# Kernel optimization log

Measured on AMD Instinct MI355X. Metric: run time of the kernel, lower is better.

## Reference

```python
import jax, jax.numpy as jnp
import numpy as np

N = 20000        # nodes
E = 640000       # edges (before self-loops)
F_IN = 128
HID = 64
HEADS = 4
F_OUT = 128
G = 64           # graphs in batch
NEG_SLOPE = 0.2  # PyG GATConv leaky_relu default


def setup_inputs() -> dict:
    key = jax.random.key(0)
    ks = jax.random.split(key, 16)
    s = 0.05
    x = jax.random.normal(ks[0], (N, F_IN), jnp.float32)
    edge_index = jax.random.randint(ks[1], (2, E), 0, N, dtype=jnp.int64)
    batch = jnp.sort(jax.random.randint(ks[2], (N,), 0, G, dtype=jnp.int64))
    # layer 1: F_IN -> HID x HEADS (concat)
    W1 = jax.random.normal(ks[3], (F_IN, HEADS * HID), jnp.float32) * s
    a_src1 = jax.random.normal(ks[4], (HEADS, HID), jnp.float32) * s
    a_dst1 = jax.random.normal(ks[5], (HEADS, HID), jnp.float32) * s
    b1 = jnp.zeros((HEADS * HID,), jnp.float32)
    # layer 2: HEADS*HID -> HID x HEADS (concat)
    W2 = jax.random.normal(ks[6], (HEADS * HID, HEADS * HID), jnp.float32) * s
    a_src2 = jax.random.normal(ks[7], (HEADS, HID), jnp.float32) * s
    a_dst2 = jax.random.normal(ks[8], (HEADS, HID), jnp.float32) * s
    b2 = jnp.zeros((HEADS * HID,), jnp.float32)
    # layer 3: HEADS*HID -> F_OUT, heads=1, concat=False (mean)
    W3 = jax.random.normal(ks[9], (HEADS * HID, F_OUT), jnp.float32) * s
    a_src3 = jax.random.normal(ks[10], (1, F_OUT), jnp.float32) * s
    a_dst3 = jax.random.normal(ks[11], (1, F_OUT), jnp.float32) * s
    b3 = jnp.zeros((F_OUT,), jnp.float32)
    return dict(x=x, edge_index=edge_index, batch=batch,
                W1=W1, a_src1=a_src1, a_dst1=a_dst1, b1=b1,
                W2=W2, a_src2=a_src2, a_dst2=a_dst2, b2=b2,
                W3=W3, a_src3=a_src3, a_dst3=a_dst3, b3=b3)


def _gat_layer(x, src, dst, W, a_s, a_d, b, heads, concat):
    n = x.shape[0]
    h = (x @ W).reshape(n, heads, -1)                # [N,H,C]
    alpha_s = (h * a_s[None]).sum(-1)                # [N,H]
    alpha_d = (h * a_d[None]).sum(-1)                # [N,H]
    e = jax.nn.leaky_relu(alpha_s[src] + alpha_d[dst], NEG_SLOPE)  # [E,H]
    # segment softmax over incoming edges of each dst node
    m = jax.ops.segment_max(e, dst, num_segments=n)
    ex = jnp.exp(e - m[dst])
    denom = jax.ops.segment_sum(ex, dst, num_segments=n)
    alpha = ex / (denom[dst] + 1e-16)                # [E,H]
    out = jax.ops.segment_sum(alpha[:, :, None] * h[src], dst, num_segments=n)  # [N,H,C]
    out = out.reshape(n, -1) if concat else out.mean(axis=1)
    return out + b


def reference(x, edge_index, batch, W1, a_src1, a_dst1, b1,
              W2, a_src2, a_dst2, b2, W3, a_src3, a_dst3, b3):
    n = x.shape[0]
    # add self loops (PyG GATConv default add_self_loops=True)
    loop = jnp.arange(n, dtype=edge_index.dtype)
    src = jnp.concatenate([edge_index[0], loop])
    dst = jnp.concatenate([edge_index[1], loop])

    h = _gat_layer(x, src, dst, W1, a_src1, a_dst1, b1, HEADS, True)
    h = jax.nn.elu(h)
    h = _gat_layer(h, src, dst, W2, a_src2, a_dst2, b2, HEADS, True)
    h = jax.nn.elu(h)
    h = _gat_layer(h, src, dst, W3, a_src3, a_dst3, b3, 1, False)

    # global mean pool over graphs
    sums = jax.ops.segment_sum(h, batch, num_segments=G)
    cnts = jax.ops.segment_sum(jnp.ones((n, 1), h.dtype), batch, num_segments=G)
    graph_embedding = sums / jnp.maximum(cnts, 1.0)
    return graph_embedding, h
```

## Files before the change

### kernel.cpp

```cpp
#include <hip/hip_runtime.h>
#include <hip/hip_bf16.h>
#include <math.h>

#define N_NODES 20000
#define N_EDGES 640000
#define ET_EDGES (N_EDGES + N_NODES)
#define G_GRAPHS 64
#define NEG_SLOPE 0.2f

typedef __attribute__((ext_vector_type(8))) short s8v;
typedef __attribute__((ext_vector_type(4))) float f4v;

__device__ __forceinline__ unsigned short bf_hi(float f) {
    union { float f; unsigned int u; } c; c.f = f;
    unsigned int r = (c.u + 0x7fffu + ((c.u >> 16) & 1u)) >> 16;
    return (unsigned short)r;
}
__device__ __forceinline__ float bf_f(unsigned short h) {
    union { unsigned int u; float f; } c; c.u = ((unsigned int)h) << 16;
    return c.f;
}


__global__ void hist_dst(const int* __restrict__ ei, int* __restrict__ cnt,
                         const int* __restrict__ batch, int* __restrict__ gstart) {
    int j = blockIdx.x * blockDim.x + threadIdx.x;
    if (blockIdx.x == 0 && threadIdx.x <= G_GRAPHS) {
        int g = threadIdx.x;
        int lo = 0, hi = N_NODES;
        while (lo < hi) {
            int mid = (lo + hi) >> 1;
            if (batch[mid] < g) lo = mid + 1; else hi = mid;
        }
        gstart[g] = lo;
    }
    if (j >= ET_EDGES) return;
    int d = (j < N_EDGES) ? ei[N_EDGES + j] : (j - N_EDGES);
    atomicAdd(&cnt[d], 1);
}

__global__ __launch_bounds__(1024) void scan_rowptr(const int* __restrict__ cnt,
                                                    int* __restrict__ row_ptr) {
    __shared__ int sums[1024];
    const int n = N_NODES;
    const int CH = (n + 1023) / 1024;
    int t = threadIdx.x;
    int base = t * CH;
    int s = 0;
    for (int i = 0; i < CH; ++i) {
        int idx = base + i;
        if (idx < n) s += cnt[idx];
    }
    sums[t] = s;
    __syncthreads();
    for (int o = 1; o < 1024; o <<= 1) {
        int v = (t >= o) ? sums[t - o] : 0;
        __syncthreads();
        sums[t] += v;
        __syncthreads();
    }
    int run = (t == 0) ? 0 : sums[t - 1];
    for (int i = 0; i < CH; ++i) {
        int idx = base + i;
        if (idx < n) { row_ptr[idx] = run; run += cnt[idx]; }
    }
    if (t == 1023) row_ptr[n] = sums[1023];
}

__global__ void fill_csr(const int* __restrict__ ei, const int* __restrict__ row_ptr,
                         int* __restrict__ cur, int* __restrict__ col) {
    int j = blockIdx.x * blockDim.x + threadIdx.x;
    if (j >= ET_EDGES) return;
    int s, d;
    if (j < N_EDGES) { s = ei[j]; d = ei[N_EDGES + j]; }
    else             { s = d = j - N_EDGES; }
    int pos = row_ptr[d] + atomicAdd(&cur[d], 1);
    col[pos] = s;
}


__global__ void prep_split(const float* __restrict__ x,
                           const float* __restrict__ W1, const float* __restrict__ W2,
                           const float* __restrict__ W3,
                           unsigned short* __restrict__ xh, unsigned short* __restrict__ xl,
                           unsigned short* __restrict__ w1h, unsigned short* __restrict__ w1l,
                           unsigned short* __restrict__ w2h, unsigned short* __restrict__ w2l,
                           unsigned short* __restrict__ w3h, unsigned short* __restrict__ w3l,
                           int* __restrict__ cntcur, float* __restrict__ gout) {
    int idx = blockIdx.x * blockDim.x + threadIdx.x;
    if (idx < 640000) {
        int i = idx * 4;
        float4 v = *(const float4*)&x[i];
        ushort4 h, l;
        h.x = bf_hi(v.x); l.x = bf_hi(v.x - bf_f(h.x));
        h.y = bf_hi(v.y); l.y = bf_hi(v.y - bf_f(h.y));
        h.z = bf_hi(v.z); l.z = bf_hi(v.z - bf_f(h.z));
        h.w = bf_hi(v.w); l.w = bf_hi(v.w - bf_f(h.w));
        *(ushort4*)&xh[i] = h;
        *(ushort4*)&xl[i] = l;
        return;
    }
    idx -= 640000;
    if (idx < 32768) {
        int k = idx / 256, n = idx % 256;
        float v = W1[idx];
        unsigned short h = bf_hi(v);
        w1h[n * 128 + k] = h;
        w1l[n * 128 + k] = bf_hi(v - bf_f(h));
        return;
    }
    idx -= 32768;
    if (idx < 65536) {
        int k = idx / 256, n = idx % 256;
        float v = W2[idx];
        unsigned short h = bf_hi(v);
        w2h[n * 256 + k] = h;
        w2l[n * 256 + k] = bf_hi(v - bf_f(h));
        return;
    }
    idx -= 65536;
    if (idx < 32768) {
        int k = idx / 128, n = idx % 128;
        float v = W3[idx];
        unsigned short h = bf_hi(v);
        w3h[n * 256 + k] = h;
        w3l[n * 256 + k] = bf_hi(v - bf_f(h));
        return;
    }
    idx -= 32768;
    if (idx < 10000) {
        *(int4*)&cntcur[idx * 4] = make_int4(0, 0, 0, 0);
        return;
    }
    idx -= 10000;
    if (idx < 2048) {
        *(float4*)&gout[idx * 4] = make_float4(0.f, 0.f, 0.f, 0.f);
    }
}


#define LDT 40

__global__ __launch_bounds__(256) void gemm_split(
        const unsigned short* __restrict__ Ah, const unsigned short* __restrict__ Al,
        const unsigned short* __restrict__ Bh, const unsigned short* __restrict__ Bl,
        float* __restrict__ C, int M, int Nc, int K) {
    __shared__ unsigned short lAh[128 * LDT];
    __shared__ unsigned short lAl[128 * LDT];
    __shared__ unsigned short lBh[64 * LDT];
    __shared__ unsigned short lBl[64 * LDT];
    int bm = blockIdx.x * 128, bn = blockIdx.y * 64;
    int t = threadIdx.x, w = t >> 6, lane = t & 63;
    int wm = (w >> 1) * 64, wn = (w & 1) * 32;

    f4v acc[4][2] = {};

    int sr = t >> 1, sk = (t & 1) << 4;
    int br = t >> 2, bk = (t & 3) << 3;
    int ar = bm + sr; if (ar >= M) ar = M - 1;
    const unsigned short* pAh = Ah + (size_t)ar * K + sk;
    const unsigned short* pAl = Al + (size_t)ar * K + sk;
    const unsigned short* pBh = Bh + (size_t)(bn + br) * K + bk;
    const unsigned short* pBl = Bl + (size_t)(bn + br) * K + bk;

    int fr = lane & 15, fk = (lane >> 4) << 3;

    for (int k0 = 0; k0 < K; k0 += 32) {
        uint4 vh0 = *(const uint4*)(pAh + k0);
        uint4 vh1 = *(const uint4*)(pAh + k0 + 8);
        uint4 vl0 = *(const uint4*)(pAl + k0);
        uint4 vl1 = *(const uint4*)(pAl + k0 + 8);
        uint4 wh  = *(const uint4*)(pBh + k0);
        uint4 wl  = *(const uint4*)(pBl + k0);
        __syncthreads();
        *(uint4*)&lAh[sr * LDT + sk]     = vh0;
        *(uint4*)&lAh[sr * LDT + sk + 8] = vh1;
        *(uint4*)&lAl[sr * LDT + sk]     = vl0;
        *(uint4*)&lAl[sr * LDT + sk + 8] = vl1;
        *(uint4*)&lBh[br * LDT + bk] = wh;
        *(uint4*)&lBl[br * LDT + bk] = wl;
        __syncthreads();

        s8v a_h[4], a_l[4], b_h[2], b_l[2];
        #pragma unroll
        for (int mi = 0; mi < 4; ++mi) {
            a_h[mi] = *(const s8v*)&lAh[(wm + mi * 16 + fr) * LDT + fk];
            a_l[mi] = *(const s8v*)&lAl[(wm + mi * 16 + fr) * LDT + fk];
        }
        #pragma unroll
        for (int nj = 0; nj < 2; ++nj) {
            b_h[nj] = *(const s8v*)&lBh[(wn + nj * 16 + fr) * LDT + fk];
            b_l[nj] = *(const s8v*)&lBl[(wn + nj * 16 + fr) * LDT + fk];
        }
        #pragma unroll
        for (int mi = 0; mi < 4; ++mi)
            #pragma unroll
            for (int nj = 0; nj < 2; ++nj) {
                acc[mi][nj] = __builtin_amdgcn_mfma_f32_16x16x32_bf16(
                    a_h[mi], b_h[nj], acc[mi][nj], 0, 0, 0);
                acc[mi][nj] = __builtin_amdgcn_mfma_f32_16x16x32_bf16(
                    a_h[mi], b_l[nj], acc[mi][nj], 0, 0, 0);
                acc[mi][nj] = __builtin_amdgcn_mfma_f32_16x16x32_bf16(
                    a_l[mi], b_h[nj], acc[mi][nj], 0, 0, 0);
            }
    }

    #pragma unroll
    for (int mi = 0; mi < 4; ++mi)
        #pragma unroll
        for (int nj = 0; nj < 2; ++nj) {
            int row0 = bm + wm + mi * 16 + (lane >> 4) * 4;
            int colc = bn + wn + nj * 16 + (lane & 15);
            #pragma unroll
            for (int q = 0; q < 4; ++q) {
                int r = row0 + q;
                if (r < M) C[(size_t)r * Nc + colc] = acc[mi][nj][q];
            }
        }
}


template <int HEADS, int C>
__global__ __launch_bounds__(256) void node_alpha2(const float* __restrict__ h,
                                                   const float* __restrict__ a_src,
                                                   const float* __restrict__ a_dst,
                                                   float* __restrict__ asT,
                                                   float* __restrict__ adT) {
    constexpr int F = HEADS * C;
    constexpr int VEC = F / 64;
    constexpr int LPH = C / VEC;
    int wid = threadIdx.x >> 6, lane = threadIdx.x & 63;
    int v = blockIdx.x * 4 + wid;
    if (v >= N_NODES) return;
    const float* hp = h + (size_t)v * F + lane * VEC;
    float ps = 0.f, pd = 0.f;
    #pragma unroll
    for (int c = 0; c < VEC; ++c) {
        float hv = hp[c];
        ps = fmaf(hv, a_src[lane * VEC + c], ps);
        pd = fmaf(hv, a_dst[lane * VEC + c], pd);
    }
    #pragma unroll
    for (int o = LPH / 2; o; o >>= 1) {
        ps += __shfl_xor(ps, o);
        pd += __shfl_xor(pd, o);
    }
    if ((lane & (LPH - 1)) == 0) {
        int head = lane / LPH;
        asT[head * N_NODES + v] = ps;
        adT[head * N_NODES + v] = pd;
    }
}


template <int SCH, int F, int HEADS, bool DO_ELU, bool SPLIT>
__global__ __launch_bounds__(256) void gat_aggregate5(
        const float* __restrict__ h,
        const float* __restrict__ asT,
        const float* __restrict__ adT,
        const int* __restrict__ row_ptr,
        const int* __restrict__ col,
        const float* __restrict__ bias,
        float* __restrict__ out,
        unsigned short* __restrict__ oh,
        unsigned short* __restrict__ ol) {
    constexpr int CL = SCH / 4;
    constexpr int E  = 64 / CL;
    constexpr int CPH = F / HEADS;
    __shared__ int2 s_po[4][64];
    int slice = blockIdx.x & 3;
    int ng = blockIdx.x >> 2;
    int wid = threadIdx.x >> 6, lane = threadIdx.x & 63;
    int v = ng * 4 + wid;
    if (v >= N_NODES) return;
    int head = (slice * SCH) / CPH;
    int eg = lane / CL, cl = lane % CL;
    int r0 = row_ptr[v], r1 = row_ptr[v + 1];
    float ad = adT[head * N_NODES + v];
    const float* asrc = asT + head * N_NODES;
    float acc[4] = {};
    float lsum = 0.f;
    const char* hbase = (const char*)h;
    unsigned laneByte = (unsigned)((slice * SCH + cl * 4) * 4);

#define GATHERN(gg, NN)                                                      \
    {                                                                        \
        int2 po[NN];                                                         \
        _Pragma("unroll")                                                    \
        for (int u = 0; u < NN; ++u) po[u] = s_po[wid][((gg) + u) * E + eg]; \
        float4 hw[NN];                                                       \
        _Pragma("unroll")                                                    \
        for (int u = 0; u < NN; ++u)                                         \
            hw[u] = *(const float4*)(hbase + (laneByte + (unsigned)po[u].x));\
        _Pragma("unroll")                                                    \
        for (int u = 0; u < NN; ++u) {                                       \
            float pk = __int_as_float(po[u].y);                              \
            acc[0] = fmaf(pk, hw[u].x, acc[0]);                              \
            acc[1] = fmaf(pk, hw[u].y, acc[1]);                              \
            acc[2] = fmaf(pk, hw[u].z, acc[2]);                              \
            acc[3] = fmaf(pk, hw[u].w, acc[3]);                              \
        }                                                                    \
    }

    for (int base = r0; base < r1; base += 64) {
        int j = base + lane;
        bool valid = j < r1;
        int s = col[valid ? j : r0];
        float e = asrc[s] + ad;
        e = (e > 0.f) ? e : NEG_SLOPE * e;
        float p = valid ? __expf(e) : 0.f;
        lsum += p;
        s_po[wid][lane] = make_int2(s * (F * 4), __float_as_int(p));

        int nk = min(64, r1 - base);
        int nkg = (nk + E - 1) / E;
        int g = 0;
        for (; g + 8 <= nkg; g += 8) GATHERN(g, 8);
        if (g + 4 <= nkg) { GATHERN(g, 4); g += 4; }
        if (g + 2 <= nkg) { GATHERN(g, 2); g += 2; }
        if (g < nkg) GATHERN(g, 1);
    }
#undef GATHERN

    #pragma unroll
    for (int o = 32; o; o >>= 1) lsum += __shfl_xor(lsum, o);
    #pragma unroll
    for (int c = 0; c < 4; ++c) {
        #pragma unroll
        for (int o = CL; o < 64; o <<= 1) acc[c] += __shfl_xor(acc[c], o);
    }
    if (eg == 0) {
        float inv = 1.f / (lsum + 1e-16f);
        int ch0 = slice * SCH + cl * 4;
        float o4[4];
        #pragma unroll
        for (int c = 0; c < 4; ++c) {
            float o = acc[c] * inv + bias[ch0 + c];
            if (DO_ELU) o = (o > 0.f) ? o : expm1f(o);
            o4[c] = o;
        }
        if constexpr (SPLIT) {
            ushort4 hv4, lv4;
            hv4.x = bf_hi(o4[0]); lv4.x = bf_hi(o4[0] - bf_f(hv4.x));
            hv4.y = bf_hi(o4[1]); lv4.y = bf_hi(o4[1] - bf_f(hv4.y));
            hv4.z = bf_hi(o4[2]); lv4.z = bf_hi(o4[2] - bf_f(hv4.z));
            hv4.w = bf_hi(o4[3]); lv4.w = bf_hi(o4[3] - bf_f(hv4.w));
            *(ushort4*)&oh[(size_t)v * F + ch0] = hv4;
            *(ushort4*)&ol[(size_t)v * F + ch0] = lv4;
        } else {
            *(float4*)&out[(size_t)v * F + ch0] =
                make_float4(o4[0], o4[1], o4[2], o4[3]);
        }
    }
}


__global__ void pool_mean4(const float* __restrict__ hout, const int* __restrict__ gstart,
                           float* __restrict__ gout) {
    int g = blockIdx.x;
    int q = blockIdx.y;
    int c = threadIdx.x;
    int off = gstart[g], end = gstart[g + 1];
    float inv = 1.f / fmaxf((float)(end - off), 1.0f);
    float s = 0.f;
    for (int i = off + q; i < end; i += 4) s += hout[(size_t)i * 128 + c];
    atomicAdd(&gout[g * 128 + c], s * inv);
}


static inline size_t align_up(size_t x, size_t a) { return (x + a - 1) & ~(a - 1); }

extern "C" void kernel_launch(void* const* d_in, const int* in_sizes, int n_in,
                              void* d_out, int out_size, void* d_ws, size_t ws_size,
                              hipStream_t stream) {
    const float* x   = (const float*)d_in[0];
    const int*   ei  = (const int*)d_in[1];
    const int*   bat = (const int*)d_in[2];
    const float* W1  = (const float*)d_in[3];
    const float* as1 = (const float*)d_in[4];
    const float* ad1 = (const float*)d_in[5];
    const float* b1  = (const float*)d_in[6];
    const float* W2  = (const float*)d_in[7];
    const float* as2 = (const float*)d_in[8];
    const float* ad2 = (const float*)d_in[9];
    const float* b2  = (const float*)d_in[10];
    const float* W3  = (const float*)d_in[11];
    const float* as3 = (const float*)d_in[12];
    const float* ad3 = (const float*)d_in[13];
    const float* b3  = (const float*)d_in[14];

    float* gout = (float*)d_out;
    float* hout = (float*)d_out + G_GRAPHS * 128;

    char* w = (char*)d_ws;
    size_t o = 0;
    float* bufA = (float*)(w + o);           o = align_up(o + (size_t)N_NODES * 256 * 4, 256);
    unsigned short* Bh = (unsigned short*)(w + o); o = align_up(o + (size_t)N_NODES * 256 * 2, 256);
    unsigned short* Bl = (unsigned short*)(w + o); o = align_up(o + (size_t)N_NODES * 256 * 2, 256);
    unsigned short* xh = (unsigned short*)(w + o); o = align_up(o + (size_t)N_NODES * 128 * 2, 256);
    unsigned short* xl = (unsigned short*)(w + o); o = align_up(o + (size_t)N_NODES * 128 * 2, 256);
    unsigned short* Wt1h = (unsigned short*)(w + o); o = align_up(o + (size_t)256 * 128 * 2, 256);
    unsigned short* Wt1l = (unsigned short*)(w + o); o = align_up(o + (size_t)256 * 128 * 2, 256);
    unsigned short* Wt2h = (unsigned short*)(w + o); o = align_up(o + (size_t)256 * 256 * 2, 256);
    unsigned short* Wt2l = (unsigned short*)(w + o); o = align_up(o + (size_t)256 * 256 * 2, 256);
    unsigned short* Wt3h = (unsigned short*)(w + o); o = align_up(o + (size_t)128 * 256 * 2, 256);
    unsigned short* Wt3l = (unsigned short*)(w + o); o = align_up(o + (size_t)128 * 256 * 2, 256);
    float* asv  = (float*)(w + o); o = align_up(o + (size_t)N_NODES * 4 * 4, 256);
    float* adv  = (float*)(w + o); o = align_up(o + (size_t)N_NODES * 4 * 4, 256);
    int* row_ptr = (int*)(w + o);  o = align_up(o + (size_t)(N_NODES + 1) * 4, 256);
    int* col     = (int*)(w + o);  o = align_up(o + (size_t)ET_EDGES * 4, 256);
    int* cnt     = (int*)(w + o);  o += (size_t)N_NODES * 4;
    int* cur     = (int*)(w + o);  o = align_up(o + (size_t)N_NODES * 4, 256);
    int* gstart  = (int*)(w + o);  o = align_up(o + (size_t)(G_GRAPHS + 1) * 4, 256);

    {
        int total = 640000 + 32768 + 65536 + 32768 + 10000 + 2048;
        prep_split<<<(total + 255) / 256, 256, 0, stream>>>(
            x, W1, W2, W3, xh, xl, Wt1h, Wt1l, Wt2h, Wt2l, Wt3h, Wt3l, cnt, gout);
    }
    hist_dst<<<(ET_EDGES + 255) / 256, 256, 0, stream>>>(ei, cnt, bat, gstart);
    scan_rowptr<<<1, 1024, 0, stream>>>(cnt, row_ptr);
    fill_csr<<<(ET_EDGES + 255) / 256, 256, 0, stream>>>(ei, row_ptr, cur, col);

    int gm = (N_NODES + 127) / 128;
    int nb = (N_NODES + 3) / 4;
    int nbs = nb * 4;

    gemm_split<<<dim3(gm, 4), 256, 0, stream>>>(xh, xl, Wt1h, Wt1l, bufA, N_NODES, 256, 128);
    node_alpha2<4, 64><<<nb, 256, 0, stream>>>(bufA, as1, ad1, asv, adv);
    gat_aggregate5<64, 256, 4, true, true><<<nbs, 256, 0, stream>>>(
        bufA, asv, adv, row_ptr, col, b1, nullptr, Bh, Bl);

    gemm_split<<<dim3(gm, 4), 256, 0, stream>>>(Bh, Bl, Wt2h, Wt2l, bufA, N_NODES, 256, 256);
    node_alpha2<4, 64><<<nb, 256, 0, stream>>>(bufA, as2, ad2, asv, adv);
    gat_aggregate5<64, 256, 4, true, true><<<nbs, 256, 0, stream>>>(
        bufA, asv, adv, row_ptr, col, b2, nullptr, Bh, Bl);

    gemm_split<<<dim3(gm, 2), 256, 0, stream>>>(Bh, Bl, Wt3h, Wt3l, bufA, N_NODES, 128, 256);
    node_alpha2<1, 128><<<nb, 256, 0, stream>>>(bufA, as3, ad3, asv, adv);
    gat_aggregate5<32, 128, 1, false, false><<<nbs, 256, 0, stream>>>(
        bufA, asv, adv, row_ptr, col, b3, hout, nullptr, nullptr);

    pool_mean4<<<dim3(G_GRAPHS, 4), 128, 0, stream>>>(hout, gstart, gout);
}
```

Before: 441.6 us.

## Fuse attention-logit dot products into GEMM epilogue and simplify gather loop

Removes the separate node_alpha kernels by computing per-node source/destination attention logits inside the GEMM epilogue. Each wave reduces its partial dot products with lane shuffles and atomically adds them into zero-initialised per-layer alpha buffers, which the prep kernel now clears. The aggregation kernel also splits the packed offset/probability shared array into two arrays and replaces the variable-width gather unroll with a fixed 4-wide gather. This saves three launches and a full re-read of the projected features, at the cost of float atomics (order-dependent rounding) and extra epilogue work.

```diff
diff --git a/kernel.cpp b/kernel.cpp
--- a/kernel.cpp
+++ b/kernel.cpp
@@ -86,7 +86,8 @@
                            unsigned short* __restrict__ w1h, unsigned short* __restrict__ w1l,
                            unsigned short* __restrict__ w2h, unsigned short* __restrict__ w2l,
                            unsigned short* __restrict__ w3h, unsigned short* __restrict__ w3l,
-                           int* __restrict__ cntcur, float* __restrict__ gout) {
+                           int* __restrict__ cntcur, float* __restrict__ gout,
+                           float* __restrict__ alphaz) {
     int idx = blockIdx.x * blockDim.x + threadIdx.x;
     if (idx < 640000) {
         int i = idx * 4;
@@ -135,16 +136,24 @@
     idx -= 10000;
     if (idx < 2048) {
         *(float4*)&gout[idx * 4] = make_float4(0.f, 0.f, 0.f, 0.f);
+        return;
+    }
+    idx -= 2048;
+    if (idx < 90000) {
+        *(float4*)&alphaz[idx * 4] = make_float4(0.f, 0.f, 0.f, 0.f);
     }
 }
 
 
 #define LDT 40
 
+template <int CPH>
 __global__ __launch_bounds__(256) void gemm_split(
         const unsigned short* __restrict__ Ah, const unsigned short* __restrict__ Al,
         const unsigned short* __restrict__ Bh, const unsigned short* __restrict__ Bl,
-        float* __restrict__ C, int M, int Nc, int K) {
+        float* __restrict__ C, int M, int Nc, int K,
+        const float* __restrict__ a_src, const float* __restrict__ a_dst,
+        float* __restrict__ asT, float* __restrict__ adT) {
     __shared__ unsigned short lAh[128 * LDT];
     __shared__ unsigned short lAl[128 * LDT];
     __shared__ unsigned short lBh[64 * LDT];
@@ -217,44 +226,40 @@
                 if (r < M) C[(size_t)r * Nc + colc] = acc[mi][nj][q];
             }
         }
-}
-
-
-template <int HEADS, int C>
-__global__ __launch_bounds__(256) void node_alpha2(const float* __restrict__ h,
-                                                   const float* __restrict__ a_src,
-                                                   const float* __restrict__ a_dst,
-                                                   float* __restrict__ asT,
-                                                   float* __restrict__ adT) {
-    constexpr int F = HEADS * C;
-    constexpr int VEC = F / 64;
-    constexpr int LPH = C / VEC;
-    int wid = threadIdx.x >> 6, lane = threadIdx.x & 63;
-    int v = blockIdx.x * 4 + wid;
-    if (v >= N_NODES) return;
-    const float* hp = h + (size_t)v * F + lane * VEC;
-    float ps = 0.f, pd = 0.f;
+
+    float av_s[2], av_d[2];
     #pragma unroll
-    for (int c = 0; c < VEC; ++c) {
-        float hv = hp[c];
-        ps = fmaf(hv, a_src[lane * VEC + c], ps);
-        pd = fmaf(hv, a_dst[lane * VEC + c], pd);
-    }
+    for (int nj = 0; nj < 2; ++nj) {
+        int aidx = bn + wn + nj * 16 + fr;
+        av_s[nj] = a_src[aidx];
+        av_d[nj] = a_dst[aidx];
+    }
+    int head = bn / CPH;
     #pragma unroll
-    for (int o = LPH / 2; o; o >>= 1) {
-        ps += __shfl_xor(ps, o);
-        pd += __shfl_xor(pd, o);
-    }
-    if ((lane & (LPH - 1)) == 0) {
-        int head = lane / LPH;
-        asT[head * N_NODES + v] = ps;
-        adT[head * N_NODES + v] = pd;
-    }
-}
-
-
-template <int SCH, int F, int HEADS, bool DO_ELU, bool SPLIT>
-__global__ __launch_bounds__(256) void gat_aggregate5(
+    for (int mi = 0; mi < 4; ++mi) {
+        #pragma unroll
+        for (int q = 0; q < 4; ++q) {
+            float ps = acc[mi][0][q] * av_s[0] + acc[mi][1][q] * av_s[1];
+            float pd = acc[mi][0][q] * av_d[0] + acc[mi][1][q] * av_d[1];
+            #pragma unroll
+            for (int o = 1; o < 16; o <<= 1) {
+                ps += __shfl_xor(ps, o);
+                pd += __shfl_xor(pd, o);
+            }
+            if (fr == 0) {
+                int r = bm + wm + mi * 16 + (lane >> 4) * 4 + q;
+                if (r < M) {
+                    atomicAdd(&asT[(size_t)head * M + r], ps);
+                    atomicAdd(&adT[(size_t)head * M + r], pd);
+                }
+            }
+        }
+    }
+}
+
+
+template <int NSLICE, int SCH, int F, int HEADS, bool DO_ELU, bool SPLIT>
+__global__ __launch_bounds__(256) void gat_aggregate_sliced(
         const float* __restrict__ h,
         const float* __restrict__ asT,
         const float* __restrict__ adT,
@@ -267,8 +272,9 @@
     constexpr int CL = SCH / 4;
     constexpr int E  = 64 / CL;
     constexpr int CPH = F / HEADS;
-    __shared__ int2 s_po[4][64];
-    int slice = blockIdx.x & 3;
+    __shared__ int   s_off[4][64];
+    __shared__ float s_p[4][64];
+    int slice = blockIdx.x & (NSLICE - 1);
     int ng = blockIdx.x >> 2;
     int wid = threadIdx.x >> 6, lane = threadIdx.x & 63;
     int v = ng * 4 + wid;
@@ -280,26 +286,38 @@
     const float* asrc = asT + head * N_NODES;
     float acc[4] = {};
     float lsum = 0.f;
-    const char* hbase = (const char*)h;
-    unsigned laneByte = (unsigned)((slice * SCH + cl * 4) * 4);
-
-#define GATHERN(gg, NN)                                                      \
-    {                                                                        \
-        int2 po[NN];                                                         \
-        _Pragma("unroll")                                                    \
-        for (int u = 0; u < NN; ++u) po[u] = s_po[wid][((gg) + u) * E + eg]; \
-        float4 hw[NN];                                                       \
-        _Pragma("unroll")                                                    \
-        for (int u = 0; u < NN; ++u)                                         \
-            hw[u] = *(const float4*)(hbase + (laneByte + (unsigned)po[u].x));\
-        _Pragma("unroll")                                                    \
-        for (int u = 0; u < NN; ++u) {                                       \
-            float pk = __int_as_float(po[u].y);                              \
-            acc[0] = fmaf(pk, hw[u].x, acc[0]);                              \
-            acc[1] = fmaf(pk, hw[u].y, acc[1]);                              \
-            acc[2] = fmaf(pk, hw[u].z, acc[2]);                              \
-            acc[3] = fmaf(pk, hw[u].w, acc[3]);                              \
-        }                                                                    \
+    const char* hb = (const char*)(h + slice * SCH + cl * 4);
+
+#define GATHER4(gg)                                                        \
+    {                                                                      \
+        int k0 = ((gg) + 0) * E + eg;                                      \
+        int k1 = ((gg) + 1) * E + eg;                                      \
+        int k2 = ((gg) + 2) * E + eg;                                      \
+        int k3 = ((gg) + 3) * E + eg;                                      \
+        float p0 = s_p[wid][k0]; int o0 = s_off[wid][k0];                  \
+        float p1 = s_p[wid][k1]; int o1 = s_off[wid][k1];                  \
+        float p2 = s_p[wid][k2]; int o2 = s_off[wid][k2];                  \
+        float p3 = s_p[wid][k3]; int o3 = s_off[wid][k3];                  \
+        float4 h0 = *(const float4*)(hb + o0);                             \
+        float4 h1 = *(const float4*)(hb + o1);                             \
+        float4 h2 = *(const float4*)(hb + o2);                             \
+        float4 h3 = *(const float4*)(hb + o3);                             \
+        acc[0] = fmaf(p0, h0.x, acc[0]);                                   \
+        acc[1] = fmaf(p0, h0.y, acc[1]);                                   \
+        acc[2] = fmaf(p0, h0.z, acc[2]);                                   \
+        acc[3] = fmaf(p0, h0.w, acc[3]);                                   \
+        acc[0] = fmaf(p1, h1.x, acc[0]);                                   \
+        acc[1] = fmaf(p1, h1.y, acc[1]);                                   \
+        acc[2] = fmaf(p1, h1.z, acc[2]);                                   \
+        acc[3] = fmaf(p1, h1.w, acc[3]);                                   \
+        acc[0] = fmaf(p2, h2.x, acc[0]);                                   \
+        acc[1] = fmaf(p2, h2.y, acc[1]);                                   \
+        acc[2] = fmaf(p2, h2.z, acc[2]);                                   \
+        acc[3] = fmaf(p2, h2.w, acc[3]);                                   \
+        acc[0] = fmaf(p3, h3.x, acc[0]);                                   \
+        acc[1] = fmaf(p3, h3.y, acc[1]);                                   \
+        acc[2] = fmaf(p3, h3.z, acc[2]);                                   \
+        acc[3] = fmaf(p3, h3.w, acc[3]);                                   \
     }
 
     for (int base = r0; base < r1; base += 64) {
@@ -310,17 +328,16 @@
         e = (e > 0.f) ? e : NEG_SLOPE * e;
         float p = valid ? __expf(e) : 0.f;
         lsum += p;
-        s_po[wid][lane] = make_int2(s * (F * 4), __float_as_int(p));
+        s_p[wid][lane] = p;
+        s_off[wid][lane] = s * (F * 4);
 
         int nk = min(64, r1 - base);
         int nkg = (nk + E - 1) / E;
         int g = 0;
-        for (; g + 8 <= nkg; g += 8) GATHERN(g, 8);
-        if (g + 4 <= nkg) { GATHERN(g, 4); g += 4; }
-        if (g + 2 <= nkg) { GATHERN(g, 2); g += 2; }
-        if (g < nkg) GATHERN(g, 1);
-    }
-#undef GATHERN
+        for (; g + 4 <= nkg; g += 4) GATHER4(g);
+        if (g < nkg) GATHER4(g);
+    }
+#undef GATHER4
 
     #pragma unroll
     for (int o = 32; o; o >>= 1) lsum += __shfl_xor(lsum, o);
@@ -405,8 +422,14 @@
     unsigned short* Wt2l = (unsigned short*)(w + o); o = align_up(o + (size_t)256 * 256 * 2, 256);
     unsigned short* Wt3h = (unsigned short*)(w + o); o = align_up(o + (size_t)128 * 256 * 2, 256);
     unsigned short* Wt3l = (unsigned short*)(w + o); o = align_up(o + (size_t)128 * 256 * 2, 256);
-    float* asv  = (float*)(w + o); o = align_up(o + (size_t)N_NODES * 4 * 4, 256);
-    float* adv  = (float*)(w + o); o = align_up(o + (size_t)N_NODES * 4 * 4, 256);
+    float* alpha = (float*)(w + o);
+    float* asv1 = alpha;
+    float* adv1 = alpha + 4 * N_NODES;
+    float* asv2 = alpha + 8 * N_NODES;
+    float* adv2 = alpha + 12 * N_NODES;
+    float* asv3 = alpha + 16 * N_NODES;
+    float* adv3 = alpha + 17 * N_NODES;
+    o = align_up(o + (size_t)18 * N_NODES * 4, 256);
     int* row_ptr = (int*)(w + o);  o = align_up(o + (size_t)(N_NODES + 1) * 4, 256);
     int* col     = (int*)(w + o);  o = align_up(o + (size_t)ET_EDGES * 4, 256);
     int* cnt     = (int*)(w + o);  o += (size_t)N_NODES * 4;
@@ -414,9 +437,9 @@
     int* gstart  = (int*)(w + o);  o = align_up(o + (size_t)(G_GRAPHS + 1) * 4, 256);
 
     {
-        int total = 640000 + 32768 + 65536 + 32768 + 10000 + 2048;
+        int total = 640000 + 32768 + 65536 + 32768 + 10000 + 2048 + 90000;
         prep_split<<<(total + 255) / 256, 256, 0, stream>>>(
-            x, W1, W2, W3, xh, xl, Wt1h, Wt1l, Wt2h, Wt2l, Wt3h, Wt3l, cnt, gout);
+            x, W1, W2, W3, xh, xl, Wt1h, Wt1l, Wt2h, Wt2l, Wt3h, Wt3l, cnt, gout, alpha);
     }
     hist_dst<<<(ET_EDGES + 255) / 256, 256, 0, stream>>>(ei, cnt, bat, gstart);
     scan_rowptr<<<1, 1024, 0, stream>>>(cnt, row_ptr);
@@ -426,20 +449,20 @@
     int nb = (N_NODES + 3) / 4;
     int nbs = nb * 4;
 
-    gemm_split<<<dim3(gm, 4), 256, 0, stream>>>(xh, xl, Wt1h, Wt1l, bufA, N_NODES, 256, 128);
-    node_alpha2<4, 64><<<nb, 256, 0, stream>>>(bufA, as1, ad1, asv, adv);
-    gat_aggregate5<64, 256, 4, true, true><<<nbs, 256, 0, stream>>>(
-        bufA, asv, adv, row_ptr, col, b1, nullptr, Bh, Bl);
-
-    gemm_split<<<dim3(gm, 4), 256, 0, stream>>>(Bh, Bl, Wt2h, Wt2l, bufA, N_NODES, 256, 256);
-    node_alpha2<4, 64><<<nb, 256, 0, stream>>>(bufA, as2, ad2, asv, adv);
-    gat_aggregate5<64, 256, 4, true, true><<<nbs, 256, 0, stream>>>(
-        bufA, asv, adv, row_ptr, col, b2, nullptr, Bh, Bl);
-
-    gemm_split<<<dim3(gm, 2), 256, 0, stream>>>(Bh, Bl, Wt3h, Wt3l, bufA, N_NODES, 128, 256);
-    node_alpha2<1, 128><<<nb, 256, 0, stream>>>(bufA, as3, ad3, asv, adv);
-    gat_aggregate5<32, 128, 1, false, false><<<nbs, 256, 0, stream>>>(
-        bufA, asv, adv, row_ptr, col, b3, hout, nullptr, nullptr);
+    gemm_split<64><<<dim3(gm, 4), 256, 0, stream>>>(
+        xh, xl, Wt1h, Wt1l, bufA, N_NODES, 256, 128, as1, ad1, asv1, adv1);
+    gat_aggregate_sliced<4, 64, 256, 4, true, true><<<nbs, 256, 0, stream>>>(
+        bufA, asv1, adv1, row_ptr, col, b1, nullptr, Bh, Bl);
+
+    gemm_split<64><<<dim3(gm, 4), 256, 0, stream>>>(
+        Bh, Bl, Wt2h, Wt2l, bufA, N_NODES, 256, 256, as2, ad2, asv2, adv2);
+    gat_aggregate_sliced<4, 64, 256, 4, true, true><<<nbs, 256, 0, stream>>>(
+        bufA, asv2, adv2, row_ptr, col, b2, nullptr, Bh, Bl);
+
+    gemm_split<128><<<dim3(gm, 2), 256, 0, stream>>>(
+        Bh, Bl, Wt3h, Wt3l, bufA, N_NODES, 128, 256, as3, ad3, asv3, adv3);
+    gat_aggregate_sliced<4, 32, 128, 1, false, false><<<nbs, 256, 0, stream>>>(
+        bufA, asv3, adv3, row_ptr, col, b3, hout, nullptr, nullptr);
 
     pool_mean4<<<dim3(G_GRAPHS, 4), 128, 0, stream>>>(hout, gstart, gout);
 }
```

New measurement: 426.0 us. -3.5%, faster.
